# Kernel tuning notes

Hardware: AMD Instinct MI355X
Metric: run time of the kernel (lower is better)

## Reference

```python
import jax, jax.numpy as jnp
import numpy as np
import math

DIM = 1024
NUM_HEADS = 16


def setup_inputs() -> dict:
    key = jax.random.key(0)
    ks = jax.random.split(key, 6)
    B, S, D = 2, 2048, DIM
    return {
        "q": jax.random.normal(ks[0], (B, S, D), dtype=jnp.float32),
        "k": jax.random.normal(ks[1], (B, S, D), dtype=jnp.float32),
        "v": jax.random.normal(ks[2], (B, S, D), dtype=jnp.float32),
        "wq": jax.random.normal(ks[3], (D, D), dtype=jnp.float32),
        "wk": jax.random.normal(ks[4], (D, D), dtype=jnp.float32),
        "wv": jax.random.normal(ks[5], (D, D), dtype=jnp.float32),
    }


def reference(q, k, v, wq, wk, wv):
    B, S, D = q.shape
    H = NUM_HEADS
    hd = D // H
    # projections: [B,S,D] @ [D,D]
    qp = (q @ wq).reshape(B, H, S, hd)  # NOTE: direct reshape, as in the original
    kp = (k @ wk).reshape(B, H, S, hd)
    vp = (v @ wv).reshape(B, H, S, hd)
    scale = 1.0 / math.sqrt(D)  # original scales by sqrt(dim), not sqrt(head_dim)
    att = jnp.einsum("bhqd,bhkd->bhqk", qp, kp) * scale  # [B,H,S,S]
    att = jax.nn.softmax(att, axis=-1)
    out = jnp.einsum("bhqk,bhkd->bhqd", att, vp)  # [B,H,S,hd]
    out = out.transpose(0, 2, 1, 3).reshape(B, S, D)
    return out
```

## Files before the change

### kernel.cpp

```cpp
#include <hip/hip_runtime.h>
#include <hip/hip_bf16.h>
#include <stdint.h>

#define DIMD 1024
#define SEQ  2048
#define NH   16
#define MROWS 4096
#define NQ   65536

typedef __bf16 bf16_t;
typedef bf16_t bf16x8 __attribute__((ext_vector_type(8)));
typedef float  f32x4  __attribute__((ext_vector_type(4)));
typedef unsigned short u16;
typedef unsigned short u16x4 __attribute__((ext_vector_type(4)));
typedef unsigned short u16x8 __attribute__((ext_vector_type(8)));
typedef unsigned int   u32;
typedef u32 u32x2 __attribute__((ext_vector_type(2)));

static __device__ __forceinline__ f32x4 mfma16(bf16x8 a, bf16x8 b, f32x4 c) {
    return __builtin_amdgcn_mfma_f32_16x16x32_bf16(a, b, c, 0, 0, 0);
}

static __device__ __forceinline__ float fast_exp2(float x) {
#if __has_builtin(__builtin_amdgcn_exp2f)
    return __builtin_amdgcn_exp2f(x);
#else
    return exp2f(x);
#endif
}

#define GLD16(gsrc, ldst) __builtin_amdgcn_global_load_lds(                    \
    (const __attribute__((address_space(1))) unsigned int*)(gsrc),             \
    (__attribute__((address_space(3))) unsigned int*)(ldst), 16, 0, 0)

static __device__ __forceinline__ void split_bf16(float x, u16& h, u16& l) {
    u32 u = __float_as_uint(x);
    u16 hu = (u16)(u >> 16);
    float xh = __uint_as_float((u32)hu << 16);
    float lo = x - xh;
    h = hu;
    l = (u16)(__float_as_uint(lo) >> 16);
}

static __device__ __forceinline__ u32 pack_bf16(float a, float b) {
    return (__float_as_uint(a) >> 16) | (__float_as_uint(b) & 0xffff0000u);
}

__global__ __launch_bounds__(256) void transWs3(
    const float* __restrict__ w0, const float* __restrict__ w1, const float* __restrict__ w2,
    u16* __restrict__ WTsH, u16* __restrict__ WTsL) {
    const int z = blockIdx.z;
    const float* W = z == 0 ? w0 : z == 1 ? w1 : w2;
    __shared__ u16 Hs[4096], Ls[4096];
    const int tid = threadIdx.x;
    const int kt = blockIdx.x, nt = blockIdx.y;
    const int n0 = nt * 128, k0 = kt * 32;
    #pragma unroll
    for (int i = 0; i < 4; i++) {
        int f = i * 256 + tid;
        int kr = f >> 5, nc4 = (f & 31) * 4;
        f32x4 w = *(const f32x4*)&W[(size_t)(k0 + kr) * DIMD + n0 + nc4];
        int cc = kr >> 3, e = kr & 7;
        #pragma unroll
        for (int j = 0; j < 4; j++) {
            u16 hh, ll; split_bf16(w[j], hh, ll);
            Hs[cc * 1024 + (nc4 + j) * 8 + e] = hh;
            Ls[cc * 1024 + (nc4 + j) * 8 + e] = ll;
        }
    }
    __syncthreads();
    const size_t base = (size_t)z * (DIMD * DIMD) + (size_t)(nt * 32 + kt) * 4096;
    #pragma unroll
    for (int i = 0; i < 2; i++) {
        int idx = (i * 256 + tid) * 8;
        *(u16x8*)(WTsH + base + idx) = *(const u16x8*)&Hs[idx];
        *(u16x8*)(WTsL + base + idx) = *(const u16x8*)&Ls[idx];
    }
}

__global__ __launch_bounds__(256, 3) void proj7(
    const float* __restrict__ xq, const float* __restrict__ xk, const float* __restrict__ xv,
    const u16* __restrict__ WTsH, const u16* __restrict__ WTsL,
    u16* __restrict__ qh, u16* __restrict__ ql,
    u16* __restrict__ kh, u16* __restrict__ kl,
    u16* __restrict__ vh) {

    const int z = blockIdx.z;
    const float* X = z == 0 ? xq : z == 1 ? xk : xv;
    const u16* BH = WTsH + (size_t)z * (DIMD * DIMD);
    const u16* BL = WTsL + (size_t)z * (DIMD * DIMD);
    u16* outH = z == 0 ? qh : z == 1 ? kh : vh;
    u16* outL = z == 0 ? ql : kl;
    const float oscale = z == 0 ? 0.0450842200278f : 1.0f;

    __shared__ u16 lds[24576];
    u16* AsH = lds;
    u16* AsL = lds + 4096;

    const int tid  = threadIdx.x;
    const int lane = tid & 63, wave = tid >> 6;
    const int quad = lane >> 4, l16 = lane & 15;
    const int wy = wave >> 1, wx = wave & 1;
    const int m0 = blockIdx.x * 128;
    const int n0 = blockIdx.y * 128;
    const size_t Bregion0 = (size_t)(blockIdx.y * 32) * 4096;

    const int rA  = tid >> 2, ccA = tid & 3;
    const int idxA0 = ccA * 1024 + ((rA ^ (ccA << 1)) * 8);
    const int idxA1 = idxA0 + 512;
    const float* Xb0 = X + (size_t)(m0 + rA) * DIMD + ccA * 8;
    const float* Xb1 = X + (size_t)(m0 + rA + 64) * DIMD + ccA * 8;

    f32x4 acc[4][4];
    #pragma unroll
    for (int mt = 0; mt < 4; mt++)
        #pragma unroll
        for (int nt = 0; nt < 4; nt++) acc[mt][nt] = (f32x4)0.0f;

    f32x4 pa0, pa1, pa2, pa3;

#define LOADA(kt) do {                                                         \
        pa0 = *(const f32x4*)(Xb0 + (kt) * 32);                                \
        pa1 = *(const f32x4*)(Xb0 + (kt) * 32 + 4);                            \
        pa2 = *(const f32x4*)(Xb1 + (kt) * 32);                                \
        pa3 = *(const f32x4*)(Xb1 + (kt) * 32 + 4);                            \
    } while (0)

#define WRITEA() do {                                                          \
        u16x8 h, l;                                                            \
        _Pragma("unroll")                                                      \
        for (int j = 0; j < 4; j++) {                                          \
            u16 hh, ll;                                                        \
            split_bf16(pa0[j], hh, ll); h[j] = hh;     l[j] = ll;              \
            split_bf16(pa1[j], hh, ll); h[4 + j] = hh; l[4 + j] = ll;          \
        }                                                                      \
        *(u16x8*)&AsH[idxA0] = h;                                              \
        *(u16x8*)&AsL[idxA0] = l;                                              \
        _Pragma("unroll")                                                      \
        for (int j = 0; j < 4; j++) {                                          \
            u16 hh, ll;                                                        \
            split_bf16(pa2[j], hh, ll); h[j] = hh;     l[j] = ll;              \
            split_bf16(pa3[j], hh, ll); h[4 + j] = hh; l[4 + j] = ll;          \
        }                                                                      \
        *(u16x8*)&AsH[idxA1] = h;                                              \
        *(u16x8*)&AsL[idxA1] = l;                                              \
    } while (0)

#define STAGEB(kt, buf) do {                                                   \
        const size_t rb = Bregion0 + (size_t)(kt) * 4096;                      \
        u16* BsHd = lds + 8192 + (buf) * 8192;                                 \
        u16* BsLd = BsHd + 4096;                                               \
        int c0 = tid, c1 = 256 + tid;                                          \
        GLD16(BH + rb + c0 * 8, &BsHd[c0 * 8]);                                \
        GLD16(BH + rb + c1 * 8, &BsHd[c1 * 8]);                                \
        GLD16(BL + rb + c0 * 8, &BsLd[c0 * 8]);                                \
        GLD16(BL + rb + c1 * 8, &BsLd[c1 * 8]);                                \
    } while (0)

    LOADA(0);
    STAGEB(0, 0);
    WRITEA();
    __syncthreads();

    for (int kt = 0; kt < 32; kt++) {
        const int cur = kt & 1;
        if (kt < 31) {
            LOADA(kt + 1);
            STAGEB(kt + 1, cur ^ 1);
        }

        const u16* BsH = lds + 8192 + cur * 8192;
        const u16* BsL = BsH + 4096;

        bf16x8 aH[4], aL[4], bH[4], bL[4];
        #pragma unroll
        for (int mt = 0; mt < 4; mt++) {
            int r = wy * 64 + mt * 16 + l16;
            int idx = quad * 1024 + ((r ^ (quad << 1)) * 8);
            aH[mt] = *(const bf16x8*)&AsH[idx];
            aL[mt] = *(const bf16x8*)&AsL[idx];
        }
        #pragma unroll
        for (int nt = 0; nt < 4; nt++) {
            int r = wx * 64 + nt * 16 + l16;
            bH[nt] = *(const bf16x8*)&BsH[(quad * 128 + r) * 8];
            bL[nt] = *(const bf16x8*)&BsL[(quad * 128 + r) * 8];
        }
        #pragma unroll
        for (int mt = 0; mt < 4; mt++)
            #pragma unroll
            for (int nt = 0; nt < 4; nt++) {
                acc[mt][nt] = mfma16(aH[mt], bH[nt], acc[mt][nt]);
                acc[mt][nt] = mfma16(aH[mt], bL[nt], acc[mt][nt]);
                acc[mt][nt] = mfma16(aL[mt], bH[nt], acc[mt][nt]);
            }

        __syncthreads();
        if (kt < 31) WRITEA();
        __syncthreads();
    }
#undef LOADA
#undef WRITEA
#undef STAGEB

    #pragma unroll
    for (int mt = 0; mt < 4; mt++)
        #pragma unroll
        for (int nt = 0; nt < 4; nt++)
            #pragma unroll
            for (int r = 0; r < 4; r++) {
                int row = m0 + wy * 64 + mt * 16 + quad * 4 + r;
                int col = n0 + wx * 64 + nt * 16 + l16;
                u16 hh, ll; split_bf16(acc[mt][nt][r] * oscale, hh, ll);
                outH[(size_t)row * DIMD + col] = hh;
                if (z != 2) outL[(size_t)row * DIMD + col] = ll;
            }
}

__global__ __launch_bounds__(256) void transposeV(
    const u16* __restrict__ vh, u16* __restrict__ vt) {
    __shared__ u16 Ls[64][72];
    const int tid = threadIdx.x;
    const int bh = blockIdx.y;
    const int s0 = blockIdx.x * 64;
    const size_t slab = (size_t)bh * (SEQ * 64);
    #pragma unroll
    for (int i = 0; i < 2; i++) {
        int f = i * 256 + tid;
        int r = f >> 3, c = (f & 7) * 8;
        int csw = c ^ (((r >> 3) & 7) << 3);
        *(u16x8*)&Ls[r][csw] = *(const u16x8*)(vh + slab + (size_t)(s0 + r) * 64 + c);
    }
    __syncthreads();
    #pragma unroll
    for (int i = 0; i < 2; i++) {
        int f = i * 256 + tid;
        int d = f >> 3, j = (f & 7) * 8;
        u16x8 o;
        #pragma unroll
        for (int jj = 0; jj < 8; jj++) {
            int rr = j + jj;
            o[jj] = Ls[rr][d ^ (((rr >> 3) & 7) << 3)];
        }
        *(u16x8*)(vt + slab + (size_t)d * SEQ + s0 + j) = o;
    }
}

__global__ __launch_bounds__(256, 3) void flash11(
    const u16* __restrict__ qh, const u16* __restrict__ ql,
    const u16* __restrict__ kh, const u16* __restrict__ kl,
    const u16* __restrict__ vt, float* __restrict__ out) {

    __shared__ u16 KH[64][72], KL[64][72], VTs[64][72];
    __shared__ u16 Ps[4][32][72];

    const int tid  = threadIdx.x;
    const int lane = tid & 63, wv = tid >> 6;
    const int quad = lane >> 4, l16 = lane & 15;
    const int bh = blockIdx.x;
    const size_t slab = (size_t)bh * (SEQ * 64);
    const int q0 = blockIdx.y * 128 + wv * 32;

    bf16x8 qfH[2][2], qfL[2][2];
    #pragma unroll
    for (int mq = 0; mq < 2; mq++) {
        const size_t rb = slab + (size_t)(q0 + mq * 16 + l16) * 64;
        #pragma unroll
        for (int kk = 0; kk < 2; kk++) {
            qfH[mq][kk] = *(const bf16x8*)(qh + rb + kk * 32 + quad * 8);
            qfL[mq][kk] = *(const bf16x8*)(ql + rb + kk * 32 + quad * 8);
        }
    }

    f32x4 O[2][4];
    float M[2] = {-3.0e38f, -3.0e38f}, L[2] = {0.0f, 0.0f};
    #pragma unroll
    for (int mq = 0; mq < 2; mq++)
        #pragma unroll
        for (int nv = 0; nv < 4; nv++) O[mq][nv] = (f32x4)0.0f;

    const int f0 = tid, f1 = 256 + tid;
    const int r0 = f0 >> 3, c0 = (f0 & 7) * 8;
    const int r1 = f1 >> 3, c1 = (f1 & 7) * 8;
    u16x8 s0, s1, s2, s3, s4, s5;

    {
        s0 = *(const u16x8*)(kh + slab + (size_t)r0 * 64 + c0);
        s1 = *(const u16x8*)(kh + slab + (size_t)r1 * 64 + c1);
        s2 = *(const u16x8*)(kl + slab + (size_t)r0 * 64 + c0);
        s3 = *(const u16x8*)(kl + slab + (size_t)r1 * 64 + c1);
        s4 = *(const u16x8*)(vt + slab + (size_t)r0 * SEQ + c0);
        s5 = *(const u16x8*)(vt + slab + (size_t)r1 * SEQ + c1);
    }
    *(u16x8*)&KH[r0][c0] = s0;  *(u16x8*)&KH[r1][c1] = s1;
    *(u16x8*)&KL[r0][c0] = s2;  *(u16x8*)&KL[r1][c1] = s3;
    *(u16x8*)&VTs[r0][c0] = s4; *(u16x8*)&VTs[r1][c1] = s5;
    __syncthreads();

    for (int t = 0; t < 32; t++) {
        if (t < 31) {
            const int j0 = (t + 1) * 64;
            s0 = *(const u16x8*)(kh + slab + (size_t)(j0 + r0) * 64 + c0);
            s1 = *(const u16x8*)(kh + slab + (size_t)(j0 + r1) * 64 + c1);
            s2 = *(const u16x8*)(kl + slab + (size_t)(j0 + r0) * 64 + c0);
            s3 = *(const u16x8*)(kl + slab + (size_t)(j0 + r1) * 64 + c1);
            s4 = *(const u16x8*)(vt + slab + (size_t)r0 * SEQ + j0 + c0);
            s5 = *(const u16x8*)(vt + slab + (size_t)r1 * SEQ + j0 + c1);
        }

        f32x4 St[2][4];
        #pragma unroll
        for (int mq = 0; mq < 2; mq++)
            #pragma unroll
            for (int nt = 0; nt < 4; nt++) St[mq][nt] = (f32x4)0.0f;
        __builtin_amdgcn_s_setprio(1);
        #pragma unroll
        for (int nt = 0; nt < 4; nt++) {
            const int rB = nt * 16 + l16;
            #pragma unroll
            for (int kk = 0; kk < 2; kk++) {
                bf16x8 kHf = *(const bf16x8*)&KH[rB][kk * 32 + quad * 8];
                bf16x8 kLf = *(const bf16x8*)&KL[rB][kk * 32 + quad * 8];
                #pragma unroll
                for (int mq = 0; mq < 2; mq++) {
                    St[mq][nt] = mfma16(kHf, qfH[mq][kk], St[mq][nt]);
                    St[mq][nt] = mfma16(kLf, qfH[mq][kk], St[mq][nt]);
                    St[mq][nt] = mfma16(kHf, qfL[mq][kk], St[mq][nt]);
                }
            }
        }
        __builtin_amdgcn_s_setprio(0);

        #pragma unroll
        for (int mq = 0; mq < 2; mq++) {
            float mx = St[mq][0][0];
            #pragma unroll
            for (int nt = 0; nt < 4; nt++)
                #pragma unroll
                for (int r = 0; r < 4; r++) mx = fmaxf(mx, St[mq][nt][r]);
            mx = fmaxf(mx, __shfl_xor(mx, 16));
            mx = fmaxf(mx, __shfl_xor(mx, 32));
            float Mn = M[mq];
            if (__any(mx > Mn)) {
                Mn = fmaxf(Mn, mx);
                float al = fast_exp2(M[mq] - Mn);
                M[mq] = Mn;
                L[mq] *= al;
                #pragma unroll
                for (int nv = 0; nv < 4; nv++) O[mq][nv] *= al;
            }
            float rs = 0.0f;
            #pragma unroll
            for (int nt = 0; nt < 4; nt++)
                #pragma unroll
                for (int r = 0; r < 4; r++) {
                    float p = fast_exp2(St[mq][nt][r] - Mn);
                    St[mq][nt][r] = p;
                    rs += p;
                }
            rs += __shfl_xor(rs, 16);
            rs += __shfl_xor(rs, 32);
            L[mq] += rs;
            #pragma unroll
            for (int nt = 0; nt < 4; nt++) {
                u32x2 d;
                d[0] = pack_bf16(St[mq][nt][0], St[mq][nt][1]);
                d[1] = pack_bf16(St[mq][nt][2], St[mq][nt][3]);
                *(u32x2*)&Ps[wv][mq * 16 + l16][nt * 16 + quad * 4] = d;
            }
        }

        __builtin_amdgcn_s_setprio(1);
        #pragma unroll
        for (int kk = 0; kk < 2; kk++) {
            bf16x8 pB[2];
            #pragma unroll
            for (int mq = 0; mq < 2; mq++)
                pB[mq] = *(const bf16x8*)&Ps[wv][mq * 16 + l16][kk * 32 + quad * 8];
            #pragma unroll
            for (int nv = 0; nv < 4; nv++) {
                bf16x8 vF = *(const bf16x8*)&VTs[nv * 16 + l16][kk * 32 + quad * 8];
                #pragma unroll
                for (int mq = 0; mq < 2; mq++)
                    O[mq][nv] = mfma16(vF, pB[mq], O[mq][nv]);
            }
        }
        __builtin_amdgcn_s_setprio(0);

        __syncthreads();
        if (t < 31) {
            *(u16x8*)&KH[r0][c0] = s0;  *(u16x8*)&KH[r1][c1] = s1;
            *(u16x8*)&KL[r0][c0] = s2;  *(u16x8*)&KL[r1][c1] = s3;
            *(u16x8*)&VTs[r0][c0] = s4; *(u16x8*)&VTs[r1][c1] = s5;
        }
        __syncthreads();
    }

    const int bb = bh >> 4, hh = bh & 15;
    #pragma unroll
    for (int mq = 0; mq < 2; mq++) {
        const int s = q0 + mq * 16 + l16;
        const float inv = 1.0f / L[mq];
        float* orow = out + ((size_t)(bb * SEQ + s)) * DIMD + hh * 64;
        #pragma unroll
        for (int nv = 0; nv < 4; nv++) {
            f32x4 o4;
            #pragma unroll
            for (int r = 0; r < 4; r++) o4[r] = O[mq][nv][r] * inv;
            *(f32x4*)(orow + nv * 16 + quad * 4) = o4;
        }
    }
}

extern "C" void kernel_launch(void* const* d_in, const int* in_sizes, int n_in,
                              void* d_out, int out_size, void* d_ws, size_t ws_size,
                              hipStream_t stream) {
    const float* q  = (const float*)d_in[0];
    const float* k  = (const float*)d_in[1];
    const float* v  = (const float*)d_in[2];
    const float* wq = (const float*)d_in[3];
    const float* wk = (const float*)d_in[4];
    const float* wv = (const float*)d_in[5];
    float* out = (float*)d_out;

    char* ws = (char*)d_ws;
    const size_t MB = 1 << 20;
    u16* qh   = (u16*)(ws + 0 * MB);
    u16* ql   = (u16*)(ws + 8 * MB);
    u16* kh   = (u16*)(ws + 16 * MB);
    u16* kl   = (u16*)(ws + 24 * MB);
    u16* vh   = (u16*)(ws + 32 * MB);
    u16* vt   = (u16*)(ws + 40 * MB);
    u16* WTsH = (u16*)(ws + 48 * MB);
    u16* WTsL = (u16*)(ws + 54 * MB);

    transWs3<<<dim3(32, 8, 3), 256, 0, stream>>>(wq, wk, wv, WTsH, WTsL);

    proj7<<<dim3(32, 8, 3), 256, 0, stream>>>(
        q, k, v, WTsH, WTsL, qh, ql, kh, kl, vh);

    transposeV<<<dim3(SEQ / 64, 2 * NH), 256, 0, stream>>>(vh, vt);

    flash11<<<dim3(2 * NH, SEQ / 128), 256, 0, stream>>>(
        qh, ql, kh, kl, vt, out);
}
```

Baseline: 249.9 us.

## Fuse V transpose into flash kernel LDS staging and relax rescale threshold

```diff
diff --git a/kernel.cpp b/kernel.cpp
--- a/kernel.cpp
+++ b/kernel.cpp
@@ -217,39 +217,10 @@
             }
 }
 
-__global__ __launch_bounds__(256) void transposeV(
-    const u16* __restrict__ vh, u16* __restrict__ vt) {
-    __shared__ u16 Ls[64][72];
-    const int tid = threadIdx.x;
-    const int bh = blockIdx.y;
-    const int s0 = blockIdx.x * 64;
-    const size_t slab = (size_t)bh * (SEQ * 64);
-    #pragma unroll
-    for (int i = 0; i < 2; i++) {
-        int f = i * 256 + tid;
-        int r = f >> 3, c = (f & 7) * 8;
-        int csw = c ^ (((r >> 3) & 7) << 3);
-        *(u16x8*)&Ls[r][csw] = *(const u16x8*)(vh + slab + (size_t)(s0 + r) * 64 + c);
-    }
-    __syncthreads();
-    #pragma unroll
-    for (int i = 0; i < 2; i++) {
-        int f = i * 256 + tid;
-        int d = f >> 3, j = (f & 7) * 8;
-        u16x8 o;
-        #pragma unroll
-        for (int jj = 0; jj < 8; jj++) {
-            int rr = j + jj;
-            o[jj] = Ls[rr][d ^ (((rr >> 3) & 7) << 3)];
-        }
-        *(u16x8*)(vt + slab + (size_t)d * SEQ + s0 + j) = o;
-    }
-}
-
-__global__ __launch_bounds__(256, 3) void flash11(
+__global__ __launch_bounds__(256, 3) void flash12(
     const u16* __restrict__ qh, const u16* __restrict__ ql,
     const u16* __restrict__ kh, const u16* __restrict__ kl,
-    const u16* __restrict__ vt, float* __restrict__ out) {
+    const u16* __restrict__ vh, float* __restrict__ out) {
 
     __shared__ u16 KH[64][72], KL[64][72], VTs[64][72];
     __shared__ u16 Ps[4][32][72];
@@ -282,19 +253,30 @@
     const int f0 = tid, f1 = 256 + tid;
     const int r0 = f0 >> 3, c0 = (f0 & 7) * 8;
     const int r1 = f1 >> 3, c1 = (f1 & 7) * 8;
+    const int vswz  = ((c0 >> 3) & 7) << 3;
+    const int vcol0 = r0 ^ vswz;
+    const int vcol1 = r1 ^ vswz;
     u16x8 s0, s1, s2, s3, s4, s5;
+
+#define STAGEV() do {                                                          \
+        _Pragma("unroll")                                                      \
+        for (int j = 0; j < 8; j++) {                                          \
+            VTs[c0 + j][vcol0] = (u16)s4[j];                                   \
+            VTs[c1 + j][vcol1] = (u16)s5[j];                                   \
+        }                                                                      \
+    } while (0)
 
     {
         s0 = *(const u16x8*)(kh + slab + (size_t)r0 * 64 + c0);
         s1 = *(const u16x8*)(kh + slab + (size_t)r1 * 64 + c1);
         s2 = *(const u16x8*)(kl + slab + (size_t)r0 * 64 + c0);
         s3 = *(const u16x8*)(kl + slab + (size_t)r1 * 64 + c1);
-        s4 = *(const u16x8*)(vt + slab + (size_t)r0 * SEQ + c0);
-        s5 = *(const u16x8*)(vt + slab + (size_t)r1 * SEQ + c1);
+        s4 = *(const u16x8*)(vh + slab + (size_t)r0 * 64 + c0);
+        s5 = *(const u16x8*)(vh + slab + (size_t)r1 * 64 + c1);
     }
     *(u16x8*)&KH[r0][c0] = s0;  *(u16x8*)&KH[r1][c1] = s1;
     *(u16x8*)&KL[r0][c0] = s2;  *(u16x8*)&KL[r1][c1] = s3;
-    *(u16x8*)&VTs[r0][c0] = s4; *(u16x8*)&VTs[r1][c1] = s5;
+    STAGEV();
     __syncthreads();
 
     for (int t = 0; t < 32; t++) {
@@ -304,8 +286,8 @@
             s1 = *(const u16x8*)(kh + slab + (size_t)(j0 + r1) * 64 + c1);
             s2 = *(const u16x8*)(kl + slab + (size_t)(j0 + r0) * 64 + c0);
             s3 = *(const u16x8*)(kl + slab + (size_t)(j0 + r1) * 64 + c1);
-            s4 = *(const u16x8*)(vt + slab + (size_t)r0 * SEQ + j0 + c0);
-            s5 = *(const u16x8*)(vt + slab + (size_t)r1 * SEQ + j0 + c1);
+            s4 = *(const u16x8*)(vh + slab + (size_t)(j0 + r0) * 64 + c0);
+            s5 = *(const u16x8*)(vh + slab + (size_t)(j0 + r1) * 64 + c1);
         }
 
         f32x4 St[2][4];
@@ -341,7 +323,7 @@
             mx = fmaxf(mx, __shfl_xor(mx, 16));
             mx = fmaxf(mx, __shfl_xor(mx, 32));
             float Mn = M[mq];
-            if (__any(mx > Mn)) {
+            if (__any(mx > Mn + 8.0f)) {
                 Mn = fmaxf(Mn, mx);
                 float al = fast_exp2(M[mq] - Mn);
                 M[mq] = Mn;
@@ -379,7 +361,9 @@
                 pB[mq] = *(const bf16x8*)&Ps[wv][mq * 16 + l16][kk * 32 + quad * 8];
             #pragma unroll
             for (int nv = 0; nv < 4; nv++) {
-                bf16x8 vF = *(const bf16x8*)&VTs[nv * 16 + l16][kk * 32 + quad * 8];
+                const int rowd = nv * 16 + l16;
+                const int colr = (kk * 32 + quad * 8) ^ ((((rowd) >> 3) & 7) << 3);
+                bf16x8 vF = *(const bf16x8*)&VTs[rowd][colr];
                 #pragma unroll
                 for (int mq = 0; mq < 2; mq++)
                     O[mq][nv] = mfma16(vF, pB[mq], O[mq][nv]);
@@ -391,10 +375,11 @@
         if (t < 31) {
             *(u16x8*)&KH[r0][c0] = s0;  *(u16x8*)&KH[r1][c1] = s1;
             *(u16x8*)&KL[r0][c0] = s2;  *(u16x8*)&KL[r1][c1] = s3;
-            *(u16x8*)&VTs[r0][c0] = s4; *(u16x8*)&VTs[r1][c1] = s5;
+            STAGEV();
         }
         __syncthreads();
     }
+#undef STAGEV
 
     const int bb = bh >> 4, hh = bh & 15;
     #pragma unroll
@@ -430,17 +415,14 @@
     u16* kh   = (u16*)(ws + 16 * MB);
     u16* kl   = (u16*)(ws + 24 * MB);
     u16* vh   = (u16*)(ws + 32 * MB);
-    u16* vt   = (u16*)(ws + 40 * MB);
-    u16* WTsH = (u16*)(ws + 48 * MB);
-    u16* WTsL = (u16*)(ws + 54 * MB);
+    u16* WTsH = (u16*)(ws + 40 * MB);
+    u16* WTsL = (u16*)(ws + 46 * MB);
 
     transWs3<<<dim3(32, 8, 3), 256, 0, stream>>>(wq, wk, wv, WTsH, WTsL);
 
     proj7<<<dim3(32, 8, 3), 256, 0, stream>>>(
         q, k, v, WTsH, WTsL, qh, ql, kh, kl, vh);
 
-    transposeV<<<dim3(SEQ / 64, 2 * NH), 256, 0, stream>>>(vh, vt);
-
-    flash11<<<dim3(2 * NH, SEQ / 128), 256, 0, stream>>>(
-        qh, ql, kh, kl, vt, out);
-}
+    flash12<<<dim3(2 * NH, SEQ / 128), 256, 0, stream>>>(
+        qh, ql, kh, kl, vh, out);
+}
```

Result: no change. 249.0 us (-0.4%).
